# Kernel optimization log

Hardware: AMD Instinct MI355X
Metric: run time of the kernel (lower is better)

## Reference

```python
import jax, jax.numpy as jnp
import numpy as np

B, N, DIM = 8, 4096, 512
H, DH = 8, 64
INNER = H * DH
MIN_FREQ = 1.0 / 64
SCALE = 1.0
ROT_DIM = DH // 2  # 32, per spatial axis
EPS = 1e-5


def setup_inputs() -> dict:
    key = jax.random.key(0)
    ks = jax.random.split(key, 6)
    x = jax.random.normal(ks[0], (B, N, DIM), dtype=jnp.float32)
    pos = jax.random.uniform(ks[1], (B, N, 2), dtype=jnp.float32)
    W_qkv = jax.random.normal(ks[2], (3 * INNER, DIM), dtype=jnp.float32) * (1.0 / DH)
    gamma_k = jnp.ones((DH,), jnp.float32)
    beta_k = jnp.zeros((DH,), jnp.float32)
    gamma_v = jnp.ones((DH,), jnp.float32)
    beta_v = jnp.zeros((DH,), jnp.float32)
    W_out = jax.random.normal(ks[3], (DIM, INNER), dtype=jnp.float32) * (1.0 / np.sqrt(INNER))
    b_out = jnp.zeros((DIM,), jnp.float32)
    return {"x": x, "pos": pos, "W_qkv": W_qkv, "gamma_k": gamma_k, "beta_k": beta_k,
            "gamma_v": gamma_v, "beta_v": beta_v, "W_out": W_out, "b_out": b_out}


def _layernorm(t, gamma, beta):
    mu = jnp.mean(t, axis=-1, keepdims=True)
    var = jnp.var(t, axis=-1, keepdims=True)
    return (t - mu) * jax.lax.rsqrt(var + EPS) * gamma + beta


def _rotate_half(t):
    # '... (j d) -> ... j d' with j=2, then cat(-x2, x1)
    d = t.shape[-1] // 2
    x1, x2 = t[..., :d], t[..., d:]
    return jnp.concatenate((-x2, x1), axis=-1)


def _apply_rot(t, freqs):
    return t * jnp.cos(freqs) + _rotate_half(t) * jnp.sin(freqs)


def _freqs(coord):
    # coord: [b, n]; inv_freq over rotary half-dim
    inv_freq = 1.0 / (10000.0 ** (jnp.arange(0, ROT_DIM, 2, dtype=jnp.float32) / ROT_DIM))
    t = coord * (SCALE / MIN_FREQ)
    f = t[..., None] * inv_freq  # [b, n, ROT_DIM//2]
    return jnp.concatenate((f, f), axis=-1)[:, None, :, :]  # [b, 1, n, ROT_DIM]


def reference(x, pos, W_qkv, gamma_k, beta_k, gamma_v, beta_v, W_out, b_out):
    b, n, _ = x.shape
    qkv = x @ W_qkv.T  # [b, n, 3*INNER]
    q, k, v = jnp.split(qkv, 3, axis=-1)
    split = lambda t: t.reshape(b, n, H, DH).transpose(0, 2, 1, 3)  # b h n d
    q, k, v = split(q), split(k), split(v)

    # Galerkin: LayerNorm on K and V over head dim
    k = _layernorm(k, gamma_k, beta_k)
    v = _layernorm(v, gamma_v, beta_v)

    # 2D rotary on q, k: first half of head dim uses x-coords, second half y-coords
    fx, fy = _freqs(pos[..., 0]), _freqs(pos[..., 1])
    rot2d = lambda t: jnp.concatenate(
        (_apply_rot(t[..., :ROT_DIM], fx), _apply_rot(t[..., ROT_DIM:], fy)), axis=-1)
    q = rot2d(q)
    k = rot2d(k)

    # Associative linear attention: (K^T V) then Q @ (.) / n
    dots = jnp.einsum('bhnd,bhne->bhde', k, v)  # [b, h, d, d]
    out = jnp.einsum('bhnd,bhde->bhne', q, dots) * (1.0 / n)
    out = out.transpose(0, 2, 1, 3).reshape(b, n, INNER)
    return out @ W_out.T + b_out
```

## Files before the change

kernel.cpp:

```cpp
#include <hip/hip_runtime.h>
#include <math.h>

#define NB 8
#define NN 4096
#define NDIM 512
#define NH 8
#define NDH 64
#define QKVC 1536
#define NROWS (NB * NN)
#define EPSF 1e-5f
#define INV_N (1.0f / 4096.0f)
#define L2_10K_16 0.8304820237218406f

typedef __bf16 bf16x8_t __attribute__((ext_vector_type(8)));
typedef float f32x4_t __attribute__((ext_vector_type(4)));
typedef unsigned short u16x8 __attribute__((ext_vector_type(8)));

__device__ inline unsigned short f2bf(float f) {
    unsigned u = __builtin_bit_cast(unsigned, f);
    u += 0x7fff + ((u >> 16) & 1);
    return (unsigned short)(u >> 16);
}
__device__ inline float bf2f(unsigned short u) {
    unsigned v = (unsigned)u << 16;
    return __builtin_bit_cast(float, v);
}

#define GLOAD_LDS16(g, s) __builtin_amdgcn_global_load_lds(                    \
    (const __attribute__((address_space(1))) void*)(g),                        \
    (__attribute__((address_space(3))) void*)(s), 16, 0, 0)

__global__ __launch_bounds__(256)
void cvt_bf16_kernel(const float* __restrict__ s, unsigned short* __restrict__ d, int n)
{
    const int i = (blockIdx.x * 256 + threadIdx.x) * 8;
    if (i >= n) return;
    float4 a = *(const float4*)(s + i);
    float4 b = *(const float4*)(s + i + 4);
    ushort4 lo, hi;
    lo.x = f2bf(a.x); lo.y = f2bf(a.y); lo.z = f2bf(a.z); lo.w = f2bf(a.w);
    hi.x = f2bf(b.x); hi.y = f2bf(b.y); hi.z = f2bf(b.z); hi.w = f2bf(b.w);
    *(ushort4*)(d + i)     = lo;
    *(ushort4*)(d + i + 4) = hi;
}

__global__ __launch_bounds__(256)
void cvt_dots_kernel(const float* __restrict__ s, unsigned short* __restrict__ d)
{
    const int i = (blockIdx.x * 256 + threadIdx.x) * 4;
    float4 a = *(const float4*)(s + i);
    ushort4 o;
    o.x = f2bf(a.x * INV_N); o.y = f2bf(a.y * INV_N);
    o.z = f2bf(a.z * INV_N); o.w = f2bf(a.w * INV_N);
    *(ushort4*)(d + i) = o;
}

__global__ __launch_bounds__(512, 2)
void gemm_qkv_fused(const unsigned short* __restrict__ A,
                    const unsigned short* __restrict__ Bm,
                    const float* __restrict__ pos,
                    const float* __restrict__ gk, const float* __restrict__ bk,
                    const float* __restrict__ gv, const float* __restrict__ bvv,
                    unsigned short* __restrict__ qb,
                    unsigned short* __restrict__ kT,
                    unsigned short* __restrict__ vT)
{
    __shared__ __align__(16) unsigned short lds[2 * 32768];

    const int tid  = threadIdx.x;
    const int wave = tid >> 6;
    const int lane = tid & 63;

    int flat = blockIdx.y * 6 + blockIdx.x;
    flat = (flat & 7) * 96 + (flat >> 3);
    const int bx = flat % 6;
    const int by = flat / 6;
    const int m0 = by * 256;
    const int n0 = bx * 256;

    const int warp_m = wave >> 2;
    const int warp_n = wave & 3;
    const int fr = lane & 15;
    const int fq = lane >> 4;
    const int ch0 = ((fq ^ (fr & 7)) << 3);
    const int ch1 = ch0 ^ 32;

    const int r6 = tid >> 3;
    const int cs = (((tid & 7) ^ (r6 & 7)) << 3);
    const unsigned short* Asrc = A  + (size_t)(m0 + r6) * NDIM + cs;
    const unsigned short* Bsrc = Bm + (size_t)(n0 + (r6 >> 5) * 64 + (r6 & 31)) * NDIM + cs;
    const int sdst = wave * 512;

#define STG_A(tt, h, c) GLOAD_LDS16(Asrc + (size_t)((c) * 128 + (h) * 64) * NDIM + (tt) * 64, \
        &lds[(((tt) & 1) << 15) + ((h) << 13) + ((c) << 12) + sdst])
#define STG_B(tt, h, c) GLOAD_LDS16(Bsrc + (size_t)((c) * 128 + (h) * 32) * NDIM + (tt) * 64, \
        &lds[(((tt) & 1) << 15) + 16384 + ((h) << 13) + ((c) << 12) + sdst])
#define VMCNT4 asm volatile("s_waitcnt vmcnt(4)" ::: "memory")
#define BARF   { __builtin_amdgcn_s_barrier(); asm volatile("" ::: "memory"); }

    f32x4_t acc[8][4] = {};

    STG_A(0, 0, 0); STG_A(0, 0, 1);
    STG_B(0, 0, 0); STG_B(0, 0, 1);
    STG_B(0, 1, 0); STG_B(0, 1, 1);
    STG_A(0, 1, 0); STG_A(0, 1, 1);

    const unsigned short* Afr = &lds[(warp_m * 64 + fr) * 64];
    const unsigned short* Bfr = &lds[16384 + (warp_n * 32 + fr) * 64];

    bf16x8_t a0[4][2], a1[4][2], b0[2][2], b1[2][2];

    for (int tt = 0; tt < 7; ++tt) {
        const int rb = (tt & 1) << 15;
        VMCNT4; BARF;
        #pragma unroll
        for (int mi = 0; mi < 4; ++mi) {
            a0[mi][0] = *(const bf16x8_t*)&Afr[rb + mi * 1024 + ch0];
            a0[mi][1] = *(const bf16x8_t*)&Afr[rb + mi * 1024 + ch1];
        }
        #pragma unroll
        for (int nj = 0; nj < 2; ++nj) {
            b0[nj][0] = *(const bf16x8_t*)&Bfr[rb + nj * 1024 + ch0];
            b0[nj][1] = *(const bf16x8_t*)&Bfr[rb + nj * 1024 + ch1];
        }
        STG_A(tt + 1, 0, 0); STG_A(tt + 1, 0, 1);
        __builtin_amdgcn_s_setprio(1);
        #pragma unroll
        for (int mi = 0; mi < 4; ++mi)
            #pragma unroll
            for (int nj = 0; nj < 2; ++nj) {
                acc[mi][nj] = __builtin_amdgcn_mfma_f32_16x16x32_bf16(a0[mi][0], b0[nj][0], acc[mi][nj], 0, 0, 0);
                acc[mi][nj] = __builtin_amdgcn_mfma_f32_16x16x32_bf16(a0[mi][1], b0[nj][1], acc[mi][nj], 0, 0, 0);
            }
        __builtin_amdgcn_s_setprio(0);
        VMCNT4; BARF;
        #pragma unroll
        for (int nj = 0; nj < 2; ++nj) {
            b1[nj][0] = *(const bf16x8_t*)&Bfr[rb + 8192 + nj * 1024 + ch0];
            b1[nj][1] = *(const bf16x8_t*)&Bfr[rb + 8192 + nj * 1024 + ch1];
        }
        STG_B(tt + 1, 0, 0); STG_B(tt + 1, 0, 1);
        __builtin_amdgcn_s_setprio(1);
        #pragma unroll
        for (int mi = 0; mi < 4; ++mi)
            #pragma unroll
            for (int nj = 0; nj < 2; ++nj) {
                acc[mi][2 + nj] = __builtin_amdgcn_mfma_f32_16x16x32_bf16(a0[mi][0], b1[nj][0], acc[mi][2 + nj], 0, 0, 0);
                acc[mi][2 + nj] = __builtin_amdgcn_mfma_f32_16x16x32_bf16(a0[mi][1], b1[nj][1], acc[mi][2 + nj], 0, 0, 0);
            }
        __builtin_amdgcn_s_setprio(0);
        VMCNT4; BARF;
        #pragma unroll
        for (int mi = 0; mi < 4; ++mi) {
            a1[mi][0] = *(const bf16x8_t*)&Afr[rb + 8192 + mi * 1024 + ch0];
            a1[mi][1] = *(const bf16x8_t*)&Afr[rb + 8192 + mi * 1024 + ch1];
        }
        STG_B(tt + 1, 1, 0); STG_B(tt + 1, 1, 1);
        __builtin_amdgcn_s_setprio(1);
        #pragma unroll
        for (int mi = 0; mi < 4; ++mi)
            #pragma unroll
            for (int nj = 0; nj < 2; ++nj) {
                acc[4 + mi][nj] = __builtin_amdgcn_mfma_f32_16x16x32_bf16(a1[mi][0], b0[nj][0], acc[4 + mi][nj], 0, 0, 0);
                acc[4 + mi][nj] = __builtin_amdgcn_mfma_f32_16x16x32_bf16(a1[mi][1], b0[nj][1], acc[4 + mi][nj], 0, 0, 0);
            }
        __builtin_amdgcn_s_setprio(0);
        STG_A(tt + 1, 1, 0); STG_A(tt + 1, 1, 1);
        __builtin_amdgcn_s_setprio(1);
        #pragma unroll
        for (int mi = 0; mi < 4; ++mi)
            #pragma unroll
            for (int nj = 0; nj < 2; ++nj) {
                acc[4 + mi][2 + nj] = __builtin_amdgcn_mfma_f32_16x16x32_bf16(a1[mi][0], b1[nj][0], acc[4 + mi][2 + nj], 0, 0, 0);
                acc[4 + mi][2 + nj] = __builtin_amdgcn_mfma_f32_16x16x32_bf16(a1[mi][1], b1[nj][1], acc[4 + mi][2 + nj], 0, 0, 0);
            }
        __builtin_amdgcn_s_setprio(0);
    }
    {
        const int rb = 32768;
        asm volatile("s_waitcnt vmcnt(0)" ::: "memory");
        BARF;
        #pragma unroll
        for (int mi = 0; mi < 4; ++mi) {
            a0[mi][0] = *(const bf16x8_t*)&Afr[rb + mi * 1024 + ch0];
            a0[mi][1] = *(const bf16x8_t*)&Afr[rb + mi * 1024 + ch1];
        }
        #pragma unroll
        for (int nj = 0; nj < 2; ++nj) {
            b0[nj][0] = *(const bf16x8_t*)&Bfr[rb + nj * 1024 + ch0];
            b0[nj][1] = *(const bf16x8_t*)&Bfr[rb + nj * 1024 + ch1];
        }
        #pragma unroll
        for (int mi = 0; mi < 4; ++mi)
            #pragma unroll
            for (int nj = 0; nj < 2; ++nj) {
                acc[mi][nj] = __builtin_amdgcn_mfma_f32_16x16x32_bf16(a0[mi][0], b0[nj][0], acc[mi][nj], 0, 0, 0);
                acc[mi][nj] = __builtin_amdgcn_mfma_f32_16x16x32_bf16(a0[mi][1], b0[nj][1], acc[mi][nj], 0, 0, 0);
            }
        #pragma unroll
        for (int nj = 0; nj < 2; ++nj) {
            b1[nj][0] = *(const bf16x8_t*)&Bfr[rb + 8192 + nj * 1024 + ch0];
            b1[nj][1] = *(const bf16x8_t*)&Bfr[rb + 8192 + nj * 1024 + ch1];
        }
        #pragma unroll
        for (int mi = 0; mi < 4; ++mi)
            #pragma unroll
            for (int nj = 0; nj < 2; ++nj) {
                acc[mi][2 + nj] = __builtin_amdgcn_mfma_f32_16x16x32_bf16(a0[mi][0], b1[nj][0], acc[mi][2 + nj], 0, 0, 0);
                acc[mi][2 + nj] = __builtin_amdgcn_mfma_f32_16x16x32_bf16(a0[mi][1], b1[nj][1], acc[mi][2 + nj], 0, 0, 0);
            }
        #pragma unroll
        for (int mi = 0; mi < 4; ++mi) {
            a1[mi][0] = *(const bf16x8_t*)&Afr[rb + 8192 + mi * 1024 + ch0];
            a1[mi][1] = *(const bf16x8_t*)&Afr[rb + 8192 + mi * 1024 + ch1];
        }
        #pragma unroll
        for (int mi = 0; mi < 4; ++mi)
            #pragma unroll
            for (int nj = 0; nj < 2; ++nj) {
                acc[4 + mi][nj] = __builtin_amdgcn_mfma_f32_16x16x32_bf16(a1[mi][0], b0[nj][0], acc[4 + mi][nj], 0, 0, 0);
                acc[4 + mi][nj] = __builtin_amdgcn_mfma_f32_16x16x32_bf16(a1[mi][1], b0[nj][1], acc[4 + mi][nj], 0, 0, 0);
                acc[4 + mi][2 + nj] = __builtin_amdgcn_mfma_f32_16x16x32_bf16(a1[mi][0], b1[nj][0], acc[4 + mi][2 + nj], 0, 0, 0);
                acc[4 + mi][2 + nj] = __builtin_amdgcn_mfma_f32_16x16x32_bf16(a1[mi][1], b1[nj][1], acc[4 + mi][2 + nj], 0, 0, 0);
            }
    }
#undef STG_A
#undef STG_B
#undef VMCNT4
#undef BARF

    const int nc = n0 + warp_n * 64;
    const int type = nc >> 9;
    const int c  = lane & 15;
    const int g4 = (lane >> 4) * 4;
    const int mrow0 = m0 + warp_m * 128;

    if (type != 0) {
        const float* gamma = (type == 1) ? gk : gv;
        const float* beta  = (type == 1) ? bk : bvv;
        float gm[4], bt[4];
        #pragma unroll
        for (int j = 0; j < 4; ++j) { gm[j] = gamma[j * 16 + c]; bt[j] = beta[j * 16 + c]; }
        #pragma unroll
        for (int i = 0; i < 8; ++i)
            #pragma unroll
            for (int r = 0; r < 4; ++r) {
                float t0 = acc[i][0][r], t1 = acc[i][1][r];
                float t2 = acc[i][2][r], t3 = acc[i][3][r];
                float s  = t0 + t1 + t2 + t3;
                float ss = t0*t0 + t1*t1 + t2*t2 + t3*t3;
                #pragma unroll
                for (int msk = 1; msk < 16; msk <<= 1) {
                    s  += __shfl_xor(s,  msk, 64);
                    ss += __shfl_xor(ss, msk, 64);
                }
                const float mu = s * (1.0f / 64.0f);
                const float rs = rsqrtf(ss * (1.0f / 64.0f) - mu * mu + EPSF);
                acc[i][0][r] = (t0 - mu) * rs * gm[0] + bt[0];
                acc[i][1][r] = (t1 - mu) * rs * gm[1] + bt[1];
                acc[i][2][r] = (t2 - mu) * rs * gm[2] + bt[2];
                acc[i][3][r] = (t3 - mu) * rs * gm[3] + bt[3];
            }
    }
    if (type != 2) {
        const float Kc = 64.0f * exp2f(-(float)c * L2_10K_16);
        #pragma unroll
        for (int i = 0; i < 8; ++i)
            #pragma unroll
            for (int r = 0; r < 4; ++r) {
                const int row = mrow0 + (i >> 2) * 64 + (i & 3) * 16 + g4 + r;
                const float2 p = ((const float2*)pos)[row];
                float sx, cx, sy, cy;
                __sincosf(p.x * Kc, &sx, &cx);
                __sincosf(p.y * Kc, &sy, &cy);
                const float t0 = acc[i][0][r], t1 = acc[i][1][r];
                const float t2 = acc[i][2][r], t3 = acc[i][3][r];
                acc[i][0][r] = t0 * cx - t1 * sx;
                acc[i][1][r] = t1 * cx + t0 * sx;
                acc[i][2][r] = t2 * cy - t3 * sy;
                acc[i][3][r] = t3 * cy + t2 * sy;
            }
    }
    if (type == 0) {
        #pragma unroll
        for (int i = 0; i < 8; ++i)
            #pragma unroll
            for (int j = 0; j < 4; ++j) {
                unsigned short* qp = qb
                    + (size_t)(mrow0 + (i >> 2) * 64 + (i & 3) * 16 + g4) * NDIM
                    + nc + j * 16 + c;
                #pragma unroll
                for (int r = 0; r < 4; ++r)
                    qp[(size_t)r * NDIM] = f2bf(acc[i][j][r]);
            }
    } else {
        unsigned short* T = (type == 1) ? kT : vT;
        const int h = (nc >> 6) & 7;
        #pragma unroll
        for (int i = 0; i < 8; ++i) {
            const int row = mrow0 + (i >> 2) * 64 + (i & 3) * 16 + g4;
            const int bb = row >> 12;
            const int nl = row & 4095;
            #pragma unroll
            for (int j = 0; j < 4; ++j) {
                ushort4 o;
                o.x = f2bf(acc[i][j][0]); o.y = f2bf(acc[i][j][1]);
                o.z = f2bf(acc[i][j][2]); o.w = f2bf(acc[i][j][3]);
                *(ushort4*)(T + ((size_t)((bb * NH + h) * 64 + j * 16 + c)) * NN + nl) = o;
            }
        }
    }
}

__global__ __launch_bounds__(256)
void dots_mfma(const unsigned short* __restrict__ kT,
               const unsigned short* __restrict__ vT,
               float* __restrict__ dots)
{
    __shared__ __align__(16) unsigned short sk[2][64 * 64];
    __shared__ __align__(16) unsigned short sv[2][64 * 64];
    const int t = threadIdx.x;
    const int w = t >> 6, l = t & 63;
    const int bh = blockIdx.z * NH + blockIdx.y;
    const int n0 = blockIdx.x * 512;

    const int r8 = l >> 3;
    const int cs = ((l & 7) ^ r8) * 8;
    const unsigned short* ksrc = kT + (size_t)(bh * 64 + w * 16 + r8) * NN + n0 + cs;
    const unsigned short* vsrc = vT + (size_t)(bh * 64 + w * 16 + r8) * NN + n0 + cs;

#define STGK(buf, kt, q) GLOAD_LDS16(ksrc + (size_t)(q) * 8 * NN + (kt), \
        &sk[buf][w * 1024 + (q) * 512])
#define STGV(buf, kt, q) GLOAD_LDS16(vsrc + (size_t)(q) * 8 * NN + (kt), \
        &sv[buf][w * 1024 + (q) * 512])

    const int fr = l & 15, fq = l >> 4;
    const int doff = (w >> 1) * 32, eoff = (w & 1) * 32;

    f32x4_t acc[2][2] = {};

    STGK(0, 0, 0); STGK(0, 0, 1); STGV(0, 0, 0); STGV(0, 0, 1);

    for (int s = 0; s < 8; ++s) {
        const int buf = s & 1;
        asm volatile("s_waitcnt vmcnt(0)" ::: "memory");
        __builtin_amdgcn_s_barrier();
        bf16x8_t ak[2][2], bv[2][2];
        #pragma unroll
        for (int di = 0; di < 2; ++di)
            #pragma unroll
            for (int ks = 0; ks < 2; ++ks)
                ak[di][ks] = *(const bf16x8_t*)
                    &sk[buf][(doff + di * 16 + fr) * 64 + (((ks * 4 + fq) ^ (fr & 7)) * 8)];
        #pragma unroll
        for (int ej = 0; ej < 2; ++ej)
            #pragma unroll
            for (int ks = 0; ks < 2; ++ks)
                bv[ej][ks] = *(const bf16x8_t*)
                    &sv[buf][(eoff + ej * 16 + fr) * 64 + (((ks * 4 + fq) ^ (fr & 7)) * 8)];
        if (s + 1 < 8) {
            const int nb = buf ^ 1, kt = (s + 1) * 64;
            STGK(nb, kt, 0); STGK(nb, kt, 1); STGV(nb, kt, 0); STGV(nb, kt, 1);
        }
        #pragma unroll
        for (int ks = 0; ks < 2; ++ks)
            #pragma unroll
            for (int di = 0; di < 2; ++di)
                #pragma unroll
                for (int ej = 0; ej < 2; ++ej)
                    acc[di][ej] = __builtin_amdgcn_mfma_f32_16x16x32_bf16(
                        ak[di][ks], bv[ej][ks], acc[di][ej], 0, 0, 0);
    }
#undef STGK
#undef STGV

    float* dp = dots + (size_t)bh * 64 * 64;
    const int cc = l & 15;
    const int rr = (l >> 4) * 4;
    #pragma unroll
    for (int di = 0; di < 2; ++di)
        #pragma unroll
        for (int ej = 0; ej < 2; ++ej)
            #pragma unroll
            for (int r = 0; r < 4; ++r)
                atomicAdd(dp + (doff + di * 16 + rr + r) * 64 + eoff + ej * 16 + cc,
                          acc[di][ej][r]);
}

__global__ __launch_bounds__(256)
void dotsw_mfma(const unsigned short* __restrict__ Woutb,
                const unsigned short* __restrict__ dots_bf,
                unsigned short* __restrict__ M2b)
{
    __shared__ unsigned short As[128 * 64];
    __shared__ unsigned short Bs[64 * 64];
    const int t = threadIdx.x;
    const int wave = t >> 6;
    const int lane = t & 63;
    const int dp0 = blockIdx.x * 128;
    const int h = blockIdx.y, b = blockIdx.z;

    const int srow = lane >> 3;
    const int scol = (lane & 7) * 8;
    const unsigned short* Ag = Woutb + (size_t)(dp0 + wave * 32 + srow) * NDIM
                             + h * NDH + scol;
    const unsigned short* Bg = dots_bf + ((size_t)(b * NH + h) * 64 + wave * 16 + srow) * 64
                             + scol;
    #pragma unroll
    for (int i = 0; i < 4; ++i)
        GLOAD_LDS16(Ag + (size_t)i * 8 * NDIM, As + wave * 2048 + i * 512);
    #pragma unroll
    for (int i = 0; i < 2; ++i)
        GLOAD_LDS16(Bg + (size_t)i * 8 * 64, Bs + wave * 1024 + i * 512);
    __syncthreads();

    const int wm = (wave >> 1) * 64;
    const int wn = (wave & 1) * 32;
    const int fr = lane & 15;
    const int fq = (lane >> 4) * 8;

    f32x4_t acc[4][2] = {};
    #pragma unroll
    for (int kk = 0; kk < 2; ++kk) {
        bf16x8_t af[4], bf[2];
        #pragma unroll
        for (int i = 0; i < 4; ++i)
            af[i] = *(const bf16x8_t*)&As[(wm + i * 16 + fr) * 64 + kk * 32 + fq];
        #pragma unroll
        for (int j = 0; j < 2; ++j)
            bf[j] = *(const bf16x8_t*)&Bs[(wn + j * 16 + fr) * 64 + kk * 32 + fq];
        #pragma unroll
        for (int i = 0; i < 4; ++i)
            #pragma unroll
            for (int j = 0; j < 2; ++j)
                acc[i][j] = __builtin_amdgcn_mfma_f32_16x16x32_bf16(
                    af[i], bf[j], acc[i][j], 0, 0, 0);
    }

    const int c  = lane & 15;
    const int g4 = (lane >> 4) * 4;
    #pragma unroll
    for (int i = 0; i < 4; ++i)
        #pragma unroll
        for (int j = 0; j < 2; ++j) {
            unsigned short* mp = M2b + ((size_t)(b * NDIM) + dp0 + wm + i * 16 + g4) * NDIM
                               + h * NDH + wn + j * 16 + c;
            #pragma unroll
            for (int r = 0; r < 4; ++r)
                mp[(size_t)r * NDIM] = f2bf(acc[i][j][r]);
        }
}

__global__ __launch_bounds__(256)
void gemm_out_mfma(const unsigned short* __restrict__ qb,
                   const unsigned short* __restrict__ M2b,
                   const float* __restrict__ bias, float* __restrict__ C)
{
    __shared__ unsigned short As[128 * 32];
    __shared__ unsigned short Bs[128 * 32];
    const int t    = threadIdx.x;
    const int wave = t >> 6;
    const int lane = t & 63;
    const int b  = blockIdx.z;
    const int m0 = b * NN + blockIdx.y * 128;
    const int n0 = blockIdx.x * 128;
    const int wm = (wave >> 1) * 64;
    const int wn = (wave & 1) * 64;
    const int K = NDIM;

    f32x4_t acc[4][4] = {};

    const int srow = wave * 32 + (lane >> 2);
    const int scol = (lane & 3) * 8;
    const unsigned short* Ag = qb + (size_t)(m0 + srow) * NDIM + scol;
    const unsigned short* Bg = M2b + ((size_t)b * NDIM + n0 + srow) * NDIM + scol;
    unsigned short* sA = As + wave * 1024;
    unsigned short* sB = Bs + wave * 1024;

    const int fr = lane & 15;
    const int fq = (lane >> 4) * 8;

    for (int kt = 0; kt < K; kt += 32) {
        __syncthreads();
        GLOAD_LDS16(Ag + kt,             sA);
        GLOAD_LDS16(Ag + kt + 16 * NDIM, sA + 512);
        GLOAD_LDS16(Bg + kt,             sB);
        GLOAD_LDS16(Bg + kt + 16 * NDIM, sB + 512);
        __syncthreads();

        bf16x8_t af[4], bf[4];
        #pragma unroll
        for (int i = 0; i < 4; ++i) {
            af[i] = *(const bf16x8_t*)&As[(wm + i * 16 + fr) * 32 + fq];
            bf[i] = *(const bf16x8_t*)&Bs[(wn + i * 16 + fr) * 32 + fq];
        }
        #pragma unroll
        for (int i = 0; i < 4; ++i)
            #pragma unroll
            for (int j = 0; j < 4; ++j)
                acc[i][j] = __builtin_amdgcn_mfma_f32_16x16x32_bf16(
                    af[i], bf[j], acc[i][j], 0, 0, 0);
    }

    const int crow = (lane >> 4) * 4;
    const int ccol = lane & 15;
    #pragma unroll
    for (int j = 0; j < 4; ++j) {
        const int cn = n0 + wn + j * 16 + ccol;
        const float bb = bias[cn];
        #pragma unroll
        for (int i = 0; i < 4; ++i) {
            float* cp = C + (size_t)(m0 + wm + i * 16 + crow) * NDIM + cn;
            #pragma unroll
            for (int r = 0; r < 4; ++r)
                cp[(size_t)r * NDIM] = acc[i][j][r] + bb;
        }
    }
}

extern "C" void kernel_launch(void* const* d_in, const int* in_sizes, int n_in,
                              void* d_out, int out_size, void* d_ws, size_t ws_size,
                              hipStream_t stream)
{
    const float* x    = (const float*)d_in[0];
    const float* pos  = (const float*)d_in[1];
    const float* Wqkv = (const float*)d_in[2];
    const float* gk   = (const float*)d_in[3];
    const float* bk   = (const float*)d_in[4];
    const float* gv   = (const float*)d_in[5];
    const float* bv   = (const float*)d_in[6];
    const float* Wout = (const float*)d_in[7];
    const float* bout = (const float*)d_in[8];
    float* out = (float*)d_out;

    float* dots = (float*)d_ws;
    unsigned short* dots_bf = (unsigned short*)(dots + (size_t)NB * NH * 64 * 64);
    unsigned short* M2b     = dots_bf + (size_t)NB * NH * 64 * 64;
    unsigned short* qb      = M2b + (size_t)NB * NDIM * NDIM;
    unsigned short* kT      = qb + (size_t)NROWS * NDIM;
    unsigned short* vT      = kT + (size_t)NB * NH * NDH * NN;
    unsigned short* xb      = vT + (size_t)NB * NH * NDH * NN;
    unsigned short* Wqkvb   = xb + (size_t)NROWS * NDIM;
    unsigned short* Woutb   = Wqkvb + (size_t)QKVC * NDIM;

    hipMemsetAsync(dots, 0, (size_t)NB * NH * 64 * 64 * sizeof(float), stream);

    dim3 blk(256);
    cvt_bf16_kernel<<<dim3(NROWS * NDIM / 2048), blk, 0, stream>>>(x, xb, NROWS * NDIM);
    cvt_bf16_kernel<<<dim3(QKVC * NDIM / 2048), blk, 0, stream>>>(Wqkv, Wqkvb, QKVC * NDIM);
    cvt_bf16_kernel<<<dim3(NDIM * NDIM / 2048), blk, 0, stream>>>(Wout, Woutb, NDIM * NDIM);
    gemm_qkv_fused<<<dim3(QKVC / 256, NROWS / 256), dim3(512), 0, stream>>>(
        xb, Wqkvb, pos, gk, bk, gv, bv, qb, kT, vT);
    dots_mfma<<<dim3(NN / 512, NH, NB), blk, 0, stream>>>(kT, vT, dots);
    cvt_dots_kernel<<<dim3(NB * NH * 64 * 64 / 1024), blk, 0, stream>>>(dots, dots_bf);
    dotsw_mfma<<<dim3(NDIM / 128, NH, NB), blk, 0, stream>>>(Woutb, dots_bf, M2b);
    gemm_out_mfma<<<dim3(NDIM / 128, NN / 128, NB), blk, 0, stream>>>(
        qb, M2b, bout, out);
}
```

Measured before the change: 285.7 us.

## Merge conversion kernels, retile QKV and output GEMMs, fold dots conversion

Replaces the three fp32-to-bf16 conversion launches and the memset with one combined kernel that also zeroes the dots buffer. The QKV GEMM moves from 256x256 tiles with a hand-scheduled quarter-step pipeline to 256x128 tiles with K=32 double buffering, a smaller LDS footprint, and higher occupancy bounds. The output GEMM is rewritten to the same 512-thread double-buffered scheme with block swizzling. The dots scaling and bf16 conversion move into the dotsw kernel's load stage, removing one kernel launch and an intermediate buffer. The trade-off is less register reuse per block in exchange for more resident waves and fewer launches.

```diff
diff --git a/kernel.cpp b/kernel.cpp
--- a/kernel.cpp
+++ b/kernel.cpp
@@ -30,11 +30,9 @@
     (const __attribute__((address_space(1))) void*)(g),                        \
     (__attribute__((address_space(3))) void*)(s), 16, 0, 0)
 
-__global__ __launch_bounds__(256)
-void cvt_bf16_kernel(const float* __restrict__ s, unsigned short* __restrict__ d, int n)
-{
-    const int i = (blockIdx.x * 256 + threadIdx.x) * 8;
-    if (i >= n) return;
+__device__ inline void cvt8v(const float* __restrict__ s,
+                             unsigned short* __restrict__ d, int i)
+{
     float4 a = *(const float4*)(s + i);
     float4 b = *(const float4*)(s + i + 4);
     ushort4 lo, hi;
@@ -45,17 +43,26 @@
 }
 
 __global__ __launch_bounds__(256)
-void cvt_dots_kernel(const float* __restrict__ s, unsigned short* __restrict__ d)
-{
-    const int i = (blockIdx.x * 256 + threadIdx.x) * 4;
-    float4 a = *(const float4*)(s + i);
-    ushort4 o;
-    o.x = f2bf(a.x * INV_N); o.y = f2bf(a.y * INV_N);
-    o.z = f2bf(a.z * INV_N); o.w = f2bf(a.w * INV_N);
-    *(ushort4*)(d + i) = o;
-}
-
-__global__ __launch_bounds__(512, 2)
+void cvt_all(const float* __restrict__ x,  const float* __restrict__ wq,
+             const float* __restrict__ wo,
+             unsigned short* __restrict__ xb, unsigned short* __restrict__ wqb,
+             unsigned short* __restrict__ wob, float* __restrict__ dots)
+{
+    const int bid = blockIdx.x, t = threadIdx.x;
+    if (bid < 8192) {
+        cvt8v(x, xb, (bid * 256 + t) * 8);
+    } else if (bid < 8576) {
+        cvt8v(wq, wqb, ((bid - 8192) * 256 + t) * 8);
+    } else if (bid < 8704) {
+        cvt8v(wo, wob, ((bid - 8576) * 256 + t) * 8);
+    } else {
+        const float4 z = {0.f, 0.f, 0.f, 0.f};
+        float4* dp = (float4*)dots + (size_t)((bid - 8704) * 256 + t) * 4;
+        dp[0] = z; dp[1] = z; dp[2] = z; dp[3] = z;
+    }
+}
+
+__global__ __launch_bounds__(512, 4)
 void gemm_qkv_fused(const unsigned short* __restrict__ A,
                     const unsigned short* __restrict__ Bm,
                     const float* __restrict__ pos,
@@ -65,175 +72,75 @@
                     unsigned short* __restrict__ kT,
                     unsigned short* __restrict__ vT)
 {
-    __shared__ __align__(16) unsigned short lds[2 * 32768];
+    __shared__ __align__(16) unsigned short lds[24576];
 
     const int tid  = threadIdx.x;
     const int wave = tid >> 6;
     const int lane = tid & 63;
 
-    int flat = blockIdx.y * 6 + blockIdx.x;
-    flat = (flat & 7) * 96 + (flat >> 3);
-    const int bx = flat % 6;
-    const int by = flat / 6;
+    int flat = blockIdx.y * 12 + blockIdx.x;
+    flat = (flat & 7) * 192 + (flat >> 3);
+    const int bx = flat % 12;
+    const int by = flat / 12;
     const int m0 = by * 256;
-    const int n0 = bx * 256;
-
-    const int warp_m = wave >> 2;
-    const int warp_n = wave & 3;
+    const int n0 = bx * 128;
+
+    const int warp_m = wave >> 1;
+    const int warp_n = wave & 1;
     const int fr = lane & 15;
     const int fq = lane >> 4;
-    const int ch0 = ((fq ^ (fr & 7)) << 3);
-    const int ch1 = ch0 ^ 32;
-
-    const int r6 = tid >> 3;
-    const int cs = (((tid & 7) ^ (r6 & 7)) << 3);
-    const unsigned short* Asrc = A  + (size_t)(m0 + r6) * NDIM + cs;
-    const unsigned short* Bsrc = Bm + (size_t)(n0 + (r6 >> 5) * 64 + (r6 & 31)) * NDIM + cs;
+    const int ch0 = ((fq ^ ((fr >> 1) & 3)) << 3);
+
+    const int rl = tid >> 2;
+    const int cs = (((tid & 3) ^ ((rl >> 1) & 3)) << 3);
+    const unsigned short* Asrc = A  + (size_t)(m0 + rl) * NDIM + cs;
+    const unsigned short* Bsrc = Bm + (size_t)(n0 + rl) * NDIM + cs;
     const int sdst = wave * 512;
 
-#define STG_A(tt, h, c) GLOAD_LDS16(Asrc + (size_t)((c) * 128 + (h) * 64) * NDIM + (tt) * 64, \
-        &lds[(((tt) & 1) << 15) + ((h) << 13) + ((c) << 12) + sdst])
-#define STG_B(tt, h, c) GLOAD_LDS16(Bsrc + (size_t)((c) * 128 + (h) * 32) * NDIM + (tt) * 64, \
-        &lds[(((tt) & 1) << 15) + 16384 + ((h) << 13) + ((c) << 12) + sdst])
-#define VMCNT4 asm volatile("s_waitcnt vmcnt(4)" ::: "memory")
+#define STG_A(tt, c) GLOAD_LDS16(Asrc + (size_t)((c) * 128) * NDIM + (tt) * 32, \
+        &lds[(((tt) & 1) * 8192) + ((c) * 4096) + sdst])
+#define STG_B(tt)    GLOAD_LDS16(Bsrc + (tt) * 32, \
+        &lds[16384 + (((tt) & 1) * 4096) + sdst])
+#define VMCNT3 asm volatile("s_waitcnt vmcnt(3)" ::: "memory")
+#define VMCNT0 asm volatile("s_waitcnt vmcnt(0)" ::: "memory")
 #define BARF   { __builtin_amdgcn_s_barrier(); asm volatile("" ::: "memory"); }
 
-    f32x4_t acc[8][4] = {};
-
-    STG_A(0, 0, 0); STG_A(0, 0, 1);
-    STG_B(0, 0, 0); STG_B(0, 0, 1);
-    STG_B(0, 1, 0); STG_B(0, 1, 1);
-    STG_A(0, 1, 0); STG_A(0, 1, 1);
-
-    const unsigned short* Afr = &lds[(warp_m * 64 + fr) * 64];
-    const unsigned short* Bfr = &lds[16384 + (warp_n * 32 + fr) * 64];
-
-    bf16x8_t a0[4][2], a1[4][2], b0[2][2], b1[2][2];
-
-    for (int tt = 0; tt < 7; ++tt) {
-        const int rb = (tt & 1) << 15;
-        VMCNT4; BARF;
-        #pragma unroll
-        for (int mi = 0; mi < 4; ++mi) {
-            a0[mi][0] = *(const bf16x8_t*)&Afr[rb + mi * 1024 + ch0];
-            a0[mi][1] = *(const bf16x8_t*)&Afr[rb + mi * 1024 + ch1];
-        }
-        #pragma unroll
-        for (int nj = 0; nj < 2; ++nj) {
-            b0[nj][0] = *(const bf16x8_t*)&Bfr[rb + nj * 1024 + ch0];
-            b0[nj][1] = *(const bf16x8_t*)&Bfr[rb + nj * 1024 + ch1];
-        }
-        STG_A(tt + 1, 0, 0); STG_A(tt + 1, 0, 1);
+    f32x4_t acc[4][4] = {};
+
+    STG_A(0, 0); STG_A(0, 1); STG_B(0);
+
+    #pragma unroll 2
+    for (int tt = 0; tt < 16; ++tt) {
+        BARF;
+        if (tt < 15) { STG_A(tt + 1, 0); STG_A(tt + 1, 1); STG_B(tt + 1); VMCNT3; }
+        else VMCNT0;
+        BARF;
+        bf16x8_t af[4], bfr[4];
+        const int ab = (tt & 1) * 8192;
+        const int bb = 16384 + (tt & 1) * 4096;
+        #pragma unroll
+        for (int mi = 0; mi < 4; ++mi)
+            af[mi] = *(const bf16x8_t*)&lds[ab + (warp_m * 64 + mi * 16 + fr) * 32 + ch0];
+        #pragma unroll
+        for (int nj = 0; nj < 4; ++nj)
+            bfr[nj] = *(const bf16x8_t*)&lds[bb + (warp_n * 64 + nj * 16 + fr) * 32 + ch0];
         __builtin_amdgcn_s_setprio(1);
         #pragma unroll
         for (int mi = 0; mi < 4; ++mi)
             #pragma unroll
-            for (int nj = 0; nj < 2; ++nj) {
-                acc[mi][nj] = __builtin_amdgcn_mfma_f32_16x16x32_bf16(a0[mi][0], b0[nj][0], acc[mi][nj], 0, 0, 0);
-                acc[mi][nj] = __builtin_amdgcn_mfma_f32_16x16x32_bf16(a0[mi][1], b0[nj][1], acc[mi][nj], 0, 0, 0);
-            }
+            for (int nj = 0; nj < 4; ++nj)
+                acc[mi][nj] = __builtin_amdgcn_mfma_f32_16x16x32_bf16(
+                    af[mi], bfr[nj], acc[mi][nj], 0, 0, 0);
         __builtin_amdgcn_s_setprio(0);
-        VMCNT4; BARF;
-        #pragma unroll
-        for (int nj = 0; nj < 2; ++nj) {
-            b1[nj][0] = *(const bf16x8_t*)&Bfr[rb + 8192 + nj * 1024 + ch0];
-            b1[nj][1] = *(const bf16x8_t*)&Bfr[rb + 8192 + nj * 1024 + ch1];
-        }
-        STG_B(tt + 1, 0, 0); STG_B(tt + 1, 0, 1);
-        __builtin_amdgcn_s_setprio(1);
-        #pragma unroll
-        for (int mi = 0; mi < 4; ++mi)
-            #pragma unroll
-            for (int nj = 0; nj < 2; ++nj) {
-                acc[mi][2 + nj] = __builtin_amdgcn_mfma_f32_16x16x32_bf16(a0[mi][0], b1[nj][0], acc[mi][2 + nj], 0, 0, 0);
-                acc[mi][2 + nj] = __builtin_amdgcn_mfma_f32_16x16x32_bf16(a0[mi][1], b1[nj][1], acc[mi][2 + nj], 0, 0, 0);
-            }
-        __builtin_amdgcn_s_setprio(0);
-        VMCNT4; BARF;
-        #pragma unroll
-        for (int mi = 0; mi < 4; ++mi) {
-            a1[mi][0] = *(const bf16x8_t*)&Afr[rb + 8192 + mi * 1024 + ch0];
-            a1[mi][1] = *(const bf16x8_t*)&Afr[rb + 8192 + mi * 1024 + ch1];
-        }
-        STG_B(tt + 1, 1, 0); STG_B(tt + 1, 1, 1);
-        __builtin_amdgcn_s_setprio(1);
-        #pragma unroll
-        for (int mi = 0; mi < 4; ++mi)
-            #pragma unroll
-            for (int nj = 0; nj < 2; ++nj) {
-                acc[4 + mi][nj] = __builtin_amdgcn_mfma_f32_16x16x32_bf16(a1[mi][0], b0[nj][0], acc[4 + mi][nj], 0, 0, 0);
-                acc[4 + mi][nj] = __builtin_amdgcn_mfma_f32_16x16x32_bf16(a1[mi][1], b0[nj][1], acc[4 + mi][nj], 0, 0, 0);
-            }
-        __builtin_amdgcn_s_setprio(0);
-        STG_A(tt + 1, 1, 0); STG_A(tt + 1, 1, 1);
-        __builtin_amdgcn_s_setprio(1);
-        #pragma unroll
-        for (int mi = 0; mi < 4; ++mi)
-            #pragma unroll
-            for (int nj = 0; nj < 2; ++nj) {
-                acc[4 + mi][2 + nj] = __builtin_amdgcn_mfma_f32_16x16x32_bf16(a1[mi][0], b1[nj][0], acc[4 + mi][2 + nj], 0, 0, 0);
-                acc[4 + mi][2 + nj] = __builtin_amdgcn_mfma_f32_16x16x32_bf16(a1[mi][1], b1[nj][1], acc[4 + mi][2 + nj], 0, 0, 0);
-            }
-        __builtin_amdgcn_s_setprio(0);
-    }
-    {
-        const int rb = 32768;
-        asm volatile("s_waitcnt vmcnt(0)" ::: "memory");
-        BARF;
-        #pragma unroll
-        for (int mi = 0; mi < 4; ++mi) {
-            a0[mi][0] = *(const bf16x8_t*)&Afr[rb + mi * 1024 + ch0];
-            a0[mi][1] = *(const bf16x8_t*)&Afr[rb + mi * 1024 + ch1];
-        }
-        #pragma unroll
-        for (int nj = 0; nj < 2; ++nj) {
-            b0[nj][0] = *(const bf16x8_t*)&Bfr[rb + nj * 1024 + ch0];
-            b0[nj][1] = *(const bf16x8_t*)&Bfr[rb + nj * 1024 + ch1];
-        }
-        #pragma unroll
-        for (int mi = 0; mi < 4; ++mi)
-            #pragma unroll
-            for (int nj = 0; nj < 2; ++nj) {
-                acc[mi][nj] = __builtin_amdgcn_mfma_f32_16x16x32_bf16(a0[mi][0], b0[nj][0], acc[mi][nj], 0, 0, 0);
-                acc[mi][nj] = __builtin_amdgcn_mfma_f32_16x16x32_bf16(a0[mi][1], b0[nj][1], acc[mi][nj], 0, 0, 0);
-            }
-        #pragma unroll
-        for (int nj = 0; nj < 2; ++nj) {
-            b1[nj][0] = *(const bf16x8_t*)&Bfr[rb + 8192 + nj * 1024 + ch0];
-            b1[nj][1] = *(const bf16x8_t*)&Bfr[rb + 8192 + nj * 1024 + ch1];
-        }
-        #pragma unroll
-        for (int mi = 0; mi < 4; ++mi)
-            #pragma unroll
-            for (int nj = 0; nj < 2; ++nj) {
-                acc[mi][2 + nj] = __builtin_amdgcn_mfma_f32_16x16x32_bf16(a0[mi][0], b1[nj][0], acc[mi][2 + nj], 0, 0, 0);
-                acc[mi][2 + nj] = __builtin_amdgcn_mfma_f32_16x16x32_bf16(a0[mi][1], b1[nj][1], acc[mi][2 + nj], 0, 0, 0);
-            }
-        #pragma unroll
-        for (int mi = 0; mi < 4; ++mi) {
-            a1[mi][0] = *(const bf16x8_t*)&Afr[rb + 8192 + mi * 1024 + ch0];
-            a1[mi][1] = *(const bf16x8_t*)&Afr[rb + 8192 + mi * 1024 + ch1];
-        }
-        #pragma unroll
-        for (int mi = 0; mi < 4; ++mi)
-            #pragma unroll
-            for (int nj = 0; nj < 2; ++nj) {
-                acc[4 + mi][nj] = __builtin_amdgcn_mfma_f32_16x16x32_bf16(a1[mi][0], b0[nj][0], acc[4 + mi][nj], 0, 0, 0);
-                acc[4 + mi][nj] = __builtin_amdgcn_mfma_f32_16x16x32_bf16(a1[mi][1], b0[nj][1], acc[4 + mi][nj], 0, 0, 0);
-                acc[4 + mi][2 + nj] = __builtin_amdgcn_mfma_f32_16x16x32_bf16(a1[mi][0], b1[nj][0], acc[4 + mi][2 + nj], 0, 0, 0);
-                acc[4 + mi][2 + nj] = __builtin_amdgcn_mfma_f32_16x16x32_bf16(a1[mi][1], b1[nj][1], acc[4 + mi][2 + nj], 0, 0, 0);
-            }
     }
 #undef STG_A
 #undef STG_B
-#undef VMCNT4
-#undef BARF
 
     const int nc = n0 + warp_n * 64;
     const int type = nc >> 9;
     const int c  = lane & 15;
     const int g4 = (lane >> 4) * 4;
-    const int mrow0 = m0 + warp_m * 128;
+    const int mrow0 = m0 + warp_m * 64;
 
     if (type != 0) {
         const float* gamma = (type == 1) ? gk : gv;
@@ -242,7 +149,7 @@
         #pragma unroll
         for (int j = 0; j < 4; ++j) { gm[j] = gamma[j * 16 + c]; bt[j] = beta[j * 16 + c]; }
         #pragma unroll
-        for (int i = 0; i < 8; ++i)
+        for (int i = 0; i < 4; ++i)
             #pragma unroll
             for (int r = 0; r < 4; ++r) {
                 float t0 = acc[i][0][r], t1 = acc[i][1][r];
@@ -265,10 +172,10 @@
     if (type != 2) {
         const float Kc = 64.0f * exp2f(-(float)c * L2_10K_16);
         #pragma unroll
-        for (int i = 0; i < 8; ++i)
+        for (int i = 0; i < 4; ++i)
             #pragma unroll
             for (int r = 0; r < 4; ++r) {
-                const int row = mrow0 + (i >> 2) * 64 + (i & 3) * 16 + g4 + r;
+                const int row = mrow0 + i * 16 + g4 + r;
                 const float2 p = ((const float2*)pos)[row];
                 float sx, cx, sy, cy;
                 __sincosf(p.x * Kc, &sx, &cx);
@@ -283,12 +190,11 @@
     }
     if (type == 0) {
         #pragma unroll
-        for (int i = 0; i < 8; ++i)
+        for (int i = 0; i < 4; ++i)
             #pragma unroll
             for (int j = 0; j < 4; ++j) {
-                unsigned short* qp = qb
-                    + (size_t)(mrow0 + (i >> 2) * 64 + (i & 3) * 16 + g4) * NDIM
-                    + nc + j * 16 + c;
+                unsigned short* qp = qb + (size_t)(mrow0 + i * 16 + g4) * NDIM
+                                   + nc + j * 16 + c;
                 #pragma unroll
                 for (int r = 0; r < 4; ++r)
                     qp[(size_t)r * NDIM] = f2bf(acc[i][j][r]);
@@ -297,8 +203,8 @@
         unsigned short* T = (type == 1) ? kT : vT;
         const int h = (nc >> 6) & 7;
         #pragma unroll
-        for (int i = 0; i < 8; ++i) {
-            const int row = mrow0 + (i >> 2) * 64 + (i & 3) * 16 + g4;
+        for (int i = 0; i < 4; ++i) {
+            const int row = mrow0 + i * 16 + g4;
             const int bb = row >> 12;
             const int nl = row & 4095;
             #pragma unroll
@@ -389,7 +295,7 @@
 
 __global__ __launch_bounds__(256)
 void dotsw_mfma(const unsigned short* __restrict__ Woutb,
-                const unsigned short* __restrict__ dots_bf,
+                const float* __restrict__ dots,
                 unsigned short* __restrict__ M2b)
 {
     __shared__ unsigned short As[128 * 64];
@@ -404,14 +310,33 @@
     const int scol = (lane & 7) * 8;
     const unsigned short* Ag = Woutb + (size_t)(dp0 + wave * 32 + srow) * NDIM
                              + h * NDH + scol;
-    const unsigned short* Bg = dots_bf + ((size_t)(b * NH + h) * 64 + wave * 16 + srow) * 64
-                             + scol;
     #pragma unroll
     for (int i = 0; i < 4; ++i)
         GLOAD_LDS16(Ag + (size_t)i * 8 * NDIM, As + wave * 2048 + i * 512);
-    #pragma unroll
-    for (int i = 0; i < 2; ++i)
-        GLOAD_LDS16(Bg + (size_t)i * 8 * 64, Bs + wave * 1024 + i * 512);
+
+    {
+        const float* Dg = dots + (size_t)(b * NH + h) * 4096;
+        const int dr = t >> 2;
+        const int dc = (t & 3) * 16;
+        const float* dgp = Dg + dr * 64 + dc;
+        float4 f0 = *(const float4*)(dgp);
+        float4 f1 = *(const float4*)(dgp + 4);
+        float4 f2 = *(const float4*)(dgp + 8);
+        float4 f3 = *(const float4*)(dgp + 12);
+        ushort4 o0, o1, o2, o3;
+        o0.x = f2bf(f0.x * INV_N); o0.y = f2bf(f0.y * INV_N);
+        o0.z = f2bf(f0.z * INV_N); o0.w = f2bf(f0.w * INV_N);
+        o1.x = f2bf(f1.x * INV_N); o1.y = f2bf(f1.y * INV_N);
+        o1.z = f2bf(f1.z * INV_N); o1.w = f2bf(f1.w * INV_N);
+        o2.x = f2bf(f2.x * INV_N); o2.y = f2bf(f2.y * INV_N);
+        o2.z = f2bf(f2.z * INV_N); o2.w = f2bf(f2.w * INV_N);
+        o3.x = f2bf(f3.x * INV_N); o3.y = f2bf(f3.y * INV_N);
+        o3.z = f2bf(f3.z * INV_N); o3.w = f2bf(f3.w * INV_N);
+        *(ushort4*)&Bs[dr * 64 + dc]      = o0;
+        *(ushort4*)&Bs[dr * 64 + dc + 4]  = o1;
+        *(ushort4*)&Bs[dr * 64 + dc + 8]  = o2;
+        *(ushort4*)&Bs[dr * 64 + dc + 12] = o3;
+    }
     __syncthreads();
 
     const int wm = (wave >> 1) * 64;
@@ -451,66 +376,86 @@
         }
 }
 
-__global__ __launch_bounds__(256)
+__global__ __launch_bounds__(512, 4)
 void gemm_out_mfma(const unsigned short* __restrict__ qb,
                    const unsigned short* __restrict__ M2b,
                    const float* __restrict__ bias, float* __restrict__ C)
 {
-    __shared__ unsigned short As[128 * 32];
-    __shared__ unsigned short Bs[128 * 32];
-    const int t    = threadIdx.x;
-    const int wave = t >> 6;
-    const int lane = t & 63;
-    const int b  = blockIdx.z;
-    const int m0 = b * NN + blockIdx.y * 128;
-    const int n0 = blockIdx.x * 128;
-    const int wm = (wave >> 1) * 64;
-    const int wn = (wave & 1) * 64;
-    const int K = NDIM;
+    __shared__ __align__(16) unsigned short lds[24576];
+
+    const int tid  = threadIdx.x;
+    const int wave = tid >> 6;
+    const int lane = tid & 63;
+
+    int flat = blockIdx.y * 4 + blockIdx.x;
+    flat = (flat & 7) * 64 + (flat >> 3);
+    const int bx = flat & 3;
+    const int by = flat >> 2;
+    const int m0 = by * 256;
+    const int n0 = bx * 128;
+    const int b  = m0 >> 12;
+
+    const int warp_m = wave >> 1;
+    const int warp_n = wave & 1;
+    const int fr = lane & 15;
+    const int fq = lane >> 4;
+    const int ch0 = ((fq ^ ((fr >> 1) & 3)) << 3);
+
+    const int rl = tid >> 2;
+    const int cs = (((tid & 3) ^ ((rl >> 1) & 3)) << 3);
+    const unsigned short* Asrc = qb + (size_t)(m0 + rl) * NDIM + cs;
+    const unsigned short* Bsrc = M2b + (size_t)b * NDIM * NDIM
+                               + (size_t)(n0 + rl) * NDIM + cs;
+    const int sdst = wave * 512;
+
+#define STG_A(tt, c) GLOAD_LDS16(Asrc + (size_t)((c) * 128) * NDIM + (tt) * 32, \
+        &lds[(((tt) & 1) * 8192) + ((c) * 4096) + sdst])
+#define STG_B(tt)    GLOAD_LDS16(Bsrc + (tt) * 32, \
+        &lds[16384 + (((tt) & 1) * 4096) + sdst])
 
     f32x4_t acc[4][4] = {};
 
-    const int srow = wave * 32 + (lane >> 2);
-    const int scol = (lane & 3) * 8;
-    const unsigned short* Ag = qb + (size_t)(m0 + srow) * NDIM + scol;
-    const unsigned short* Bg = M2b + ((size_t)b * NDIM + n0 + srow) * NDIM + scol;
-    unsigned short* sA = As + wave * 1024;
-    unsigned short* sB = Bs + wave * 1024;
-
-    const int fr = lane & 15;
-    const int fq = (lane >> 4) * 8;
-
-    for (int kt = 0; kt < K; kt += 32) {
-        __syncthreads();
-        GLOAD_LDS16(Ag + kt,             sA);
-        GLOAD_LDS16(Ag + kt + 16 * NDIM, sA + 512);
-        GLOAD_LDS16(Bg + kt,             sB);
-        GLOAD_LDS16(Bg + kt + 16 * NDIM, sB + 512);
-        __syncthreads();
-
-        bf16x8_t af[4], bf[4];
-        #pragma unroll
-        for (int i = 0; i < 4; ++i) {
-            af[i] = *(const bf16x8_t*)&As[(wm + i * 16 + fr) * 32 + fq];
-            bf[i] = *(const bf16x8_t*)&Bs[(wn + i * 16 + fr) * 32 + fq];
-        }
-        #pragma unroll
-        for (int i = 0; i < 4; ++i)
-            #pragma unroll
-            for (int j = 0; j < 4; ++j)
-                acc[i][j] = __builtin_amdgcn_mfma_f32_16x16x32_bf16(
-                    af[i], bf[j], acc[i][j], 0, 0, 0);
-    }
-
-    const int crow = (lane >> 4) * 4;
-    const int ccol = lane & 15;
+    STG_A(0, 0); STG_A(0, 1); STG_B(0);
+
+    #pragma unroll 2
+    for (int tt = 0; tt < 16; ++tt) {
+        BARF;
+        if (tt < 15) { STG_A(tt + 1, 0); STG_A(tt + 1, 1); STG_B(tt + 1); VMCNT3; }
+        else VMCNT0;
+        BARF;
+        bf16x8_t af[4], bfr[4];
+        const int ab = (tt & 1) * 8192;
+        const int bb = 16384 + (tt & 1) * 4096;
+        #pragma unroll
+        for (int mi = 0; mi < 4; ++mi)
+            af[mi] = *(const bf16x8_t*)&lds[ab + (warp_m * 64 + mi * 16 + fr) * 32 + ch0];
+        #pragma unroll
+        for (int nj = 0; nj < 4; ++nj)
+            bfr[nj] = *(const bf16x8_t*)&lds[bb + (warp_n * 64 + nj * 16 + fr) * 32 + ch0];
+        __builtin_amdgcn_s_setprio(1);
+        #pragma unroll
+        for (int mi = 0; mi < 4; ++mi)
+            #pragma unroll
+            for (int nj = 0; nj < 4; ++nj)
+                acc[mi][nj] = __builtin_amdgcn_mfma_f32_16x16x32_bf16(
+                    af[mi], bfr[nj], acc[mi][nj], 0, 0, 0);
+        __builtin_amdgcn_s_setprio(0);
+    }
+#undef STG_A
+#undef STG_B
+
+    const int c  = lane & 15;
+    const int g4 = (lane >> 4) * 4;
+    const int mrow0 = m0 + warp_m * 64;
+    const int ncol = n0 + warp_n * 64;
+
     #pragma unroll
     for (int j = 0; j < 4; ++j) {
-        const int cn = n0 + wn + j * 16 + ccol;
-        const float bb = bias[cn];
+        const int col = ncol + j * 16 + c;
+        const float bb = bias[col];
         #pragma unroll
         for (int i = 0; i < 4; ++i) {
-            float* cp = C + (size_t)(m0 + wm + i * 16 + crow) * NDIM + cn;
+            float* cp = C + (size_t)(mrow0 + i * 16 + g4) * NDIM + col;
             #pragma unroll
             for (int r = 0; r < 4; ++r)
                 cp[(size_t)r * NDIM] = acc[i][j][r] + bb;
@@ -534,8 +479,7 @@
     float* out = (float*)d_out;
 
     float* dots = (float*)d_ws;
-    unsigned short* dots_bf = (unsigned short*)(dots + (size_t)NB * NH * 64 * 64);
-    unsigned short* M2b     = dots_bf + (size_t)NB * NH * 64 * 64;
+    unsigned short* M2b     = (unsigned short*)(dots + (size_t)NB * NH * 64 * 64);
     unsigned short* qb      = M2b + (size_t)NB * NDIM * NDIM;
     unsigned short* kT      = qb + (size_t)NROWS * NDIM;
     unsigned short* vT      = kT + (size_t)NB * NH * NDH * NN;
@@ -543,17 +487,11 @@
     unsigned short* Wqkvb   = xb + (size_t)NROWS * NDIM;
     unsigned short* Woutb   = Wqkvb + (size_t)QKVC * NDIM;
 
-    hipMemsetAsync(dots, 0, (size_t)NB * NH * 64 * 64 * sizeof(float), stream);
-
-    dim3 blk(256);
-    cvt_bf16_kernel<<<dim3(NROWS * NDIM / 2048), blk, 0, stream>>>(x, xb, NROWS * NDIM);
-    cvt_bf16_kernel<<<dim3(QKVC * NDIM / 2048), blk, 0, stream>>>(Wqkv, Wqkvb, QKVC * NDIM);
-    cvt_bf16_kernel<<<dim3(NDIM * NDIM / 2048), blk, 0, stream>>>(Wout, Woutb, NDIM * NDIM);
-    gemm_qkv_fused<<<dim3(QKVC / 256, NROWS / 256), dim3(512), 0, stream>>>(
+    cvt_all<<<dim3(8768), dim3(256), 0, stream>>>(x, Wqkv, Wout, xb, Wqkvb, Woutb, dots);
+    gemm_qkv_fused<<<dim3(QKVC / 128, NROWS / 256), dim3(512), 0, stream>>>(
         xb, Wqkvb, pos, gk, bk, gv, bv, qb, kT, vT);
-    dots_mfma<<<dim3(NN / 512, NH, NB), blk, 0, stream>>>(kT, vT, dots);
-    cvt_dots_kernel<<<dim3(NB * NH * 64 * 64 / 1024), blk, 0, stream>>>(dots, dots_bf);
-    dotsw_mfma<<<dim3(NDIM / 128, NH, NB), blk, 0, stream>>>(Woutb, dots_bf, M2b);
-    gemm_out_mfma<<<dim3(NDIM / 128, NN / 128, NB), blk, 0, stream>>>(
+    dots_mfma<<<dim3(NN / 512, NH, NB), dim3(256), 0, stream>>>(kT, vT, dots);
+    dotsw_mfma<<<dim3(NDIM / 128, NH, NB), dim3(256), 0, stream>>>(Woutb, dots, M2b);
+    gemm_out_mfma<<<dim3(NDIM / 128, NROWS / 256), dim3(512), 0, stream>>>(
         qb, M2b, bout, out);
 }
```

New measurement: 266.3 us. 6.8% less time.
